# Kernel optimization log

Hardware: AMD Instinct MI355X
Metric: run time of the kernel (lower is better)

## Reference

```python
import jax, jax.numpy as jnp
import numpy as np

T, B, V, D, H, C = 2048, 32, 50257, 512, 768, 10


def setup_inputs() -> dict:
    key = jax.random.key(0)
    ks = jax.random.split(key, 11)
    s = 0.02
    return {
        "x": jax.random.randint(ks[0], (T, B), 0, V),
        "embed_table": jax.random.normal(ks[1], (V, D), jnp.float32) * s,
        "W_x": jax.random.normal(ks[2], (H, D), jnp.float32) * s,
        "W_f": jax.random.normal(ks[3], (H, D), jnp.float32) * s,
        "b_f": jax.random.normal(ks[4], (H,), jnp.float32) * s,
        "W_r": jax.random.normal(ks[5], (H, D), jnp.float32) * s,
        "b_r": jax.random.normal(ks[6], (H,), jnp.float32) * s,
        "W_cx": jax.random.normal(ks[7], (H, D), jnp.float32) * s,
        "b_cx": jax.random.normal(ks[8], (H,), jnp.float32) * s,
        "W_out": jax.random.normal(ks[9], (C, H), jnp.float32) * s,
        "b_out": jax.random.normal(ks[10], (C,), jnp.float32) * s,
    }


def reference(x, embed_table, W_x, W_f, b_f, W_r, b_r, W_cx, b_cx, W_out, b_out):
    # Embedding lookup: [T, B, D]
    e = embed_table[x]
    # Precompute all gate projections for every timestep (batched GEMMs).
    xp = jnp.einsum("tbd,hd->tbh", e, W_x)                 # x_t projection
    f = jax.nn.sigmoid(jnp.einsum("tbd,hd->tbh", e, W_f) + b_f)   # forget gate
    r = jax.nn.sigmoid(jnp.einsum("tbd,hd->tbh", e, W_r) + b_r)   # reset gate
    cx = jnp.einsum("tbd,hd->tbh", e, W_cx) + b_cx                # highway path

    c0 = jnp.zeros((B, H), e.dtype)  # init_hidden: zeros

    def step(c, inp):
        f_t, xp_t, r_t, cx_t = inp
        c = f_t * c + (1.0 - f_t) * xp_t
        h = r_t * jnp.tanh(c) + (1.0 - r_t) * cx_t
        return c, h

    _, ht = jax.lax.scan(step, c0, (f, xp, r, cx))  # ht: [T, B, H]

    # tanh -> max-pool over time -> tanh -> classifier
    pooled = jnp.max(jnp.tanh(ht), axis=0)          # [B, H]
    pooled = jnp.tanh(pooled)
    logit = pooled @ W_out.T + b_out                # [B, C]
    return logit
```

## Files before the change

### kernel.cpp

```cpp
#include <hip/hip_runtime.h>
#include <hip/hip_bf16.h>
#include <cstdint>
#include <cstddef>

#define T_DIM 2048
#define B_DIM 32
#define D_DIM 512
#define H_DIM 768
#define C_DIM 10
#define K_DIM D_DIM
#define N_DIM (4 * H_DIM)

#define TC 1024
#define NCHUNK (T_DIM / TC)
#define MC (TC * B_DIM)

#define L_SEG 64
#define S_SEG (TC / L_SEG)
#define BH (B_DIM * H_DIM)

typedef __attribute__((ext_vector_type(8))) short short8;
typedef __attribute__((ext_vector_type(4))) float float4v;

__device__ inline unsigned short f2bf(float f) {
  unsigned int u = __builtin_bit_cast(unsigned int, f);
  unsigned int r = (u + 0x7FFFu + ((u >> 16) & 1u)) >> 16;
  return (unsigned short)r;
}
__device__ inline float bf2f(unsigned short s) {
  unsigned int u = ((unsigned int)s) << 16;
  return __builtin_bit_cast(float, u);
}
__device__ inline float fast_rcp(float x) { return __builtin_amdgcn_rcpf(x); }
__device__ inline float fast_exp2(float x) { return __builtin_amdgcn_exp2f(x); }
__device__ inline float sigmoid_f(float x) {
  float e = fast_exp2(-1.4426950408889634f * x);
  return fast_rcp(1.0f + e);
}
__device__ inline float tanh_f(float x) {
  float e = fast_exp2(2.885390081777927f * x);
  return 1.0f - 2.0f * fast_rcp(e + 1.0f);
}
__device__ inline void gld16(const unsigned short* g, unsigned short* l) {
  __builtin_amdgcn_global_load_lds(
      (const __attribute__((address_space(1))) void*)g,
      (__attribute__((address_space(3))) void*)l, 16, 0, 0);
}

__global__ __launch_bounds__(256) void gather_embed_kernel(
    const int* __restrict__ x_c, const float* __restrict__ table,
    unsigned short* __restrict__ ebfc) {
  int idx = blockIdx.x * 256 + threadIdx.x;
  int m = idx >> 7;
  int k4 = (idx & 127) << 2;
  int row = x_c[m];
  float4 v = *(const float4*)(table + (size_t)row * D_DIM + k4);
  ushort4 o;
  o.x = f2bf(v.x); o.y = f2bf(v.y); o.z = f2bf(v.z); o.w = f2bf(v.w);
  *(ushort4*)(ebfc + (size_t)m * D_DIM + k4) = o;
}

__global__ __launch_bounds__(256) void convert_w_kernel(
    const float* __restrict__ Wx, const float* __restrict__ Wf,
    const float* __restrict__ Wr, const float* __restrict__ Wcx,
    unsigned short* __restrict__ wcat) {
  int idx = blockIdx.x * 256 + threadIdx.x;
  int n = idx >> 7;
  int k4 = (idx & 127) << 2;
  int mat = n / H_DIM;
  int h = n - mat * H_DIM;
  const float* src = (mat == 0) ? Wx : (mat == 1) ? Wf : (mat == 2) ? Wr : Wcx;
  float4 v = *(const float4*)(src + (size_t)h * D_DIM + k4);
  ushort4 o;
  o.x = f2bf(v.x); o.y = f2bf(v.y); o.z = f2bf(v.z); o.w = f2bf(v.w);
  *(ushort4*)(wcat + (size_t)n * D_DIM + k4) = o;
}

#define BM 128
#define BN 128
#define BK 32

__global__ __launch_bounds__(256) void gemm_kernel(
    const unsigned short* __restrict__ ebfc,
    const unsigned short* __restrict__ wcat,
    const float* __restrict__ b_f, const float* __restrict__ b_r,
    const float* __restrict__ b_cx,
    unsigned short* __restrict__ projc) {
  __shared__ __align__(16) unsigned short smem[17408];
  unsigned short* As0 = smem;
  unsigned short* As1 = smem + 4096;
  unsigned short* Bs0 = smem + 8192;
  unsigned short* Bs1 = smem + 12288;

  int tid  = threadIdx.x;
  int wave = tid >> 6;
  int lane = tid & 63;
  int quad = lane >> 4;
  int l16  = lane & 15;
  int m0 = blockIdx.y * BM;
  int n0 = blockIdx.x * BN;
  int wm = (wave >> 1) * 64;
  int wn = (wave & 1) * 64;

  int row0 = tid >> 2;
  int cl0  = (tid & 3) ^ ((row0 >> 1) & 3);
  int row1 = 64 + row0;
  int cl1  = (tid & 3) ^ ((row1 >> 1) & 3);

  float4v acc[4][4] = {};

#define STAGE(Adst, Bdst, kt) do { \
    gld16(ebfc + (size_t)(m0 + row0) * K_DIM + (kt) + cl0 * 8, (Adst) + tid * 8); \
    gld16(wcat + (size_t)(n0 + row0) * K_DIM + (kt) + cl0 * 8, (Bdst) + tid * 8); \
    gld16(ebfc + (size_t)(m0 + row1) * K_DIM + (kt) + cl1 * 8, (Adst) + 2048 + tid * 8); \
    gld16(wcat + (size_t)(n0 + row1) * K_DIM + (kt) + cl1 * 8, (Bdst) + 2048 + tid * 8); } while (0)

  STAGE(As0, Bs0, 0);
  __syncthreads();

  for (int ki = 0; ki < K_DIM / BK; ki++) {
    unsigned short* Ac = (ki & 1) ? As1 : As0;
    unsigned short* Bc = (ki & 1) ? Bs1 : Bs0;
    if (ki + 1 < K_DIM / BK) {
      unsigned short* An = (ki & 1) ? As0 : As1;
      unsigned short* Bn = (ki & 1) ? Bs0 : Bs1;
      STAGE(An, Bn, (ki + 1) * BK);
    }
    short8 af[4], bfr[4];
#pragma unroll
    for (int i = 0; i < 4; i++) {
      int r = wm + i * 16 + l16;
      int p = quad ^ ((r >> 1) & 3);
      af[i] = *(const short8*)(Ac + r * BK + p * 8);
    }
#pragma unroll
    for (int j = 0; j < 4; j++) {
      int r = wn + j * 16 + l16;
      int p = quad ^ ((r >> 1) & 3);
      bfr[j] = *(const short8*)(Bc + r * BK + p * 8);
    }
#pragma unroll
    for (int i = 0; i < 4; i++)
#pragma unroll
      for (int j = 0; j < 4; j++)
        acc[i][j] = __builtin_amdgcn_mfma_f32_16x16x32_bf16(af[i], bfr[j], acc[i][j], 0, 0, 0);
    __syncthreads();
  }

  int mat = n0 / H_DIM;
  const float* bias = (mat == 1) ? b_f : (mat == 2) ? b_r : b_cx;
#pragma unroll
  for (int i = 0; i < 4; i++) {
    int row = wm + i * 16 + quad * 4;
#pragma unroll
    for (int j = 0; j < 4; j++) {
      int col = wn + j * 16 + l16;
      int h = n0 + col - mat * H_DIM;
      float bv = (mat == 0) ? 0.0f : bias[h];
#pragma unroll
      for (int r = 0; r < 4; r++) {
        float v = acc[i][j][r] + bv;
        if (mat == 1 || mat == 2) v = sigmoid_f(v);
        smem[(row + r) * 136 + col] = f2bf(v);
      }
    }
  }
  __syncthreads();
  size_t matBase = (size_t)mat * MC * H_DIM;
  int hb = n0 - mat * H_DIM;
#pragma unroll
  for (int s = 0; s < 8; s++) {
    int idx = s * 256 + tid;
    int row = idx >> 4;
    int col8 = (idx & 15) * 8;
    short8 v = *(const short8*)(smem + row * 136 + col8);
    *(short8*)(projc + matBase + (size_t)(m0 + row) * H_DIM + hb + col8) = v;
  }
}

__global__ __launch_bounds__(128) void scan1_kernel(
    const unsigned short* __restrict__ projc,
    float* __restrict__ Pw, float* __restrict__ Qw) {
  int blk = blockIdx.x;
  int seg = blk / (B_DIM * 3);
  int rem = blk % (B_DIM * 3);
  int b = rem / 3, hc = rem % 3;
  int h = hc * 256 + threadIdx.x * 2;
  const size_t mstr = (size_t)MC * H_DIM;
  size_t idx0 = ((size_t)(seg * L_SEG) * B_DIM + b) * H_DIM + h;
  float p0 = 1.f, p1 = 1.f, c0 = 0.f, c1 = 0.f;
#pragma unroll 4
  for (int t = 0; t < L_SEG; t++) {
    size_t id = idx0 + (size_t)t * BH;
    ushort2 xp = *(const ushort2*)(projc + id);
    ushort2 ff = *(const ushort2*)(projc + mstr + id);
    float f0 = bf2f(ff.x), f1 = bf2f(ff.y);
    float x0 = bf2f(xp.x), x1 = bf2f(xp.y);
    c0 = fmaf(f0, c0 - x0, x0);
    c1 = fmaf(f1, c1 - x1, x1);
    p0 *= f0; p1 *= f1;
  }
  int o = seg * BH + b * H_DIM + h;
  *(float2*)(Pw + o) = make_float2(p0, p1);
  *(float2*)(Qw + o) = make_float2(c0, c1);
}

__global__ __launch_bounds__(256) void prefix_kernel(
    const float* __restrict__ Pw, const float* __restrict__ Qw,
    float* __restrict__ cin, float* __restrict__ c_state,
    const float* __restrict__ segmax, float* __restrict__ hm_state,
    int first, int hm_init) {
  int gid = blockIdx.x * 256 + threadIdx.x;
  float c = first ? 0.f : c_state[gid];
#pragma unroll
  for (int s = 0; s < S_SEG; s++) {
    cin[s * BH + gid] = c;
    c = fmaf(Pw[s * BH + gid], c, Qw[s * BH + gid]);
  }
  c_state[gid] = c;
  if (!first) {
    float m = segmax[gid];
#pragma unroll
    for (int s = 1; s < S_SEG; s++) m = fmaxf(m, segmax[s * BH + gid]);
    hm_state[gid] = hm_init ? m : fmaxf(hm_state[gid], m);
  }
}

__global__ __launch_bounds__(128) void scan2_kernel(
    const unsigned short* __restrict__ projc,
    const float* __restrict__ cin, float* __restrict__ segmax) {
  int blk = blockIdx.x;
  int seg = blk / (B_DIM * 3);
  int rem = blk % (B_DIM * 3);
  int b = rem / 3, hc = rem % 3;
  int h = hc * 256 + threadIdx.x * 2;
  const size_t mstr = (size_t)MC * H_DIM;
  size_t idx0 = ((size_t)(seg * L_SEG) * B_DIM + b) * H_DIM + h;
  int o = seg * BH + b * H_DIM + h;
  float2 cv = *(const float2*)(cin + o);
  float c0 = cv.x, c1 = cv.y, m0 = -1e30f, m1 = -1e30f;
#pragma unroll 4
  for (int t = 0; t < L_SEG; t++) {
    size_t id = idx0 + (size_t)t * BH;
    ushort2 xp = *(const ushort2*)(projc + id);
    ushort2 ff = *(const ushort2*)(projc + mstr + id);
    ushort2 rr = *(const ushort2*)(projc + 2 * mstr + id);
    ushort2 cx = *(const ushort2*)(projc + 3 * mstr + id);
    float f0 = bf2f(ff.x), f1 = bf2f(ff.y);
    float x0 = bf2f(xp.x), x1 = bf2f(xp.y);
    float r0 = bf2f(rr.x), r1 = bf2f(rr.y);
    float g0 = bf2f(cx.x), g1 = bf2f(cx.y);
    c0 = fmaf(f0, c0 - x0, x0);
    c1 = fmaf(f1, c1 - x1, x1);
    float h0 = fmaf(r0, tanh_f(c0) - g0, g0);
    float h1 = fmaf(r1, tanh_f(c1) - g1, g1);
    m0 = fmaxf(m0, h0); m1 = fmaxf(m1, h1);
  }
  *(float2*)(segmax + o) = make_float2(m0, m1);
}

__global__ __launch_bounds__(256) void pool_final_kernel(
    const float* __restrict__ segmax, const float* __restrict__ hm_state,
    float* __restrict__ pooled) {
  int gid = blockIdx.x * 256 + threadIdx.x;
  float m = hm_state[gid];
#pragma unroll
  for (int s = 0; s < S_SEG; s++) m = fmaxf(m, segmax[s * BH + gid]);
  pooled[gid] = tanh_f(tanh_f(m));
}

__global__ __launch_bounds__(64) void classifier_kernel(
    const float* __restrict__ pooled, const float* __restrict__ W_out,
    const float* __restrict__ b_out, float* __restrict__ out) {
  int b = blockIdx.x / C_DIM;
  int c = blockIdx.x % C_DIM;
  int lane = threadIdx.x;
  float s = 0.0f;
#pragma unroll
  for (int i = 0; i < H_DIM / 64; i++) {
    int h = i * 64 + lane;
    s += pooled[(size_t)b * H_DIM + h] * W_out[(size_t)c * H_DIM + h];
  }
#pragma unroll
  for (int off = 32; off; off >>= 1) s += __shfl_down(s, off, 64);
  if (lane == 0) out[b * C_DIM + c] = s + b_out[c];
}

extern "C" void kernel_launch(void* const* d_in, const int* in_sizes, int n_in,
                              void* d_out, int out_size, void* d_ws, size_t ws_size,
                              hipStream_t stream) {
  const int*   x     = (const int*)d_in[0];
  const float* table = (const float*)d_in[1];
  const float* W_x   = (const float*)d_in[2];
  const float* W_f   = (const float*)d_in[3];
  const float* b_f   = (const float*)d_in[4];
  const float* W_r   = (const float*)d_in[5];
  const float* b_r   = (const float*)d_in[6];
  const float* W_cx  = (const float*)d_in[7];
  const float* b_cx  = (const float*)d_in[8];
  const float* W_out = (const float*)d_in[9];
  const float* b_out = (const float*)d_in[10];

  char* ws = (char*)d_ws;
  size_t off = 0;
  unsigned short* wcat  = (unsigned short*)(ws + off); off += (size_t)N_DIM * K_DIM * 2;
  unsigned short* ebfc  = (unsigned short*)(ws + off); off += (size_t)MC * K_DIM * 2;
  unsigned short* projc = (unsigned short*)(ws + off); off += (size_t)4 * MC * H_DIM * 2;
  float* Pw     = (float*)(ws + off); off += (size_t)S_SEG * BH * 4;
  float* Qw     = (float*)(ws + off); off += (size_t)S_SEG * BH * 4;
  float* cin    = (float*)(ws + off); off += (size_t)S_SEG * BH * 4;
  float* segmax = (float*)(ws + off); off += (size_t)S_SEG * BH * 4;
  float* c_st   = (float*)(ws + off); off += (size_t)BH * 4;
  float* hm_st  = (float*)(ws + off); off += (size_t)BH * 4;
  float* pooled = (float*)(ws + off); off += (size_t)BH * 4;

  convert_w_kernel<<<(N_DIM * K_DIM / 4) / 256, 256, 0, stream>>>(W_x, W_f, W_r, W_cx, wcat);

  dim3 g(N_DIM / BN, MC / BM);
  for (int ch = 0; ch < NCHUNK; ch++) {
    gather_embed_kernel<<<(MC * K_DIM / 4) / 256, 256, 0, stream>>>(x + (size_t)ch * MC, table, ebfc);
    gemm_kernel<<<g, 256, 0, stream>>>(ebfc, wcat, b_f, b_r, b_cx, projc);
    scan1_kernel<<<S_SEG * B_DIM * 3, 128, 0, stream>>>(projc, Pw, Qw);
    prefix_kernel<<<BH / 256, 256, 0, stream>>>(Pw, Qw, cin, c_st, segmax, hm_st,
                                                ch == 0, ch == 1);
    scan2_kernel<<<S_SEG * B_DIM * 3, 128, 0, stream>>>(projc, cin, segmax);
  }
  pool_final_kernel<<<BH / 256, 256, 0, stream>>>(segmax, hm_st, pooled);
  classifier_kernel<<<B_DIM * C_DIM, 64, 0, stream>>>(pooled, W_out, b_out, (float*)d_out);
}
```

Before: 604.1 us.

## Swap MFMA operands for direct packed epilogue stores; widen scan kernels to 4 elements

The GEMM now feeds the weights as the MFMA A operand and the embeddings as B, so each lane's accumulator holds four consecutive h values. The epilogue can then add a float4 bias, apply the sigmoid and write packed 8-byte bf16 stores straight to global memory, with no LDS staging pass or extra barrier. The K loop is fully unrolled with precomputed global pointers. Both scan kernels now process four contiguous elements per thread using 8-byte loads, which halves the grid size. The direct stores are only 8 bytes and strided across rows, so they may coalesce worse than the old 16-byte row-contiguous writes.

```diff
diff --git a/kernel.cpp b/kernel.cpp
--- a/kernel.cpp
+++ b/kernel.cpp
@@ -45,6 +45,9 @@
   __builtin_amdgcn_global_load_lds(
       (const __attribute__((address_space(1))) void*)g,
       (__attribute__((address_space(3))) void*)l, 16, 0, 0);
+}
+__device__ inline unsigned int pack_bf16x2(float lo, float hi) {
+  return ((unsigned int)f2bf(hi) << 16) | (unsigned int)f2bf(lo);
 }
 
 __global__ __launch_bounds__(256) void gather_embed_kernel(
@@ -86,11 +89,8 @@
     const float* __restrict__ b_f, const float* __restrict__ b_r,
     const float* __restrict__ b_cx,
     unsigned short* __restrict__ projc) {
-  __shared__ __align__(16) unsigned short smem[17408];
-  unsigned short* As0 = smem;
-  unsigned short* As1 = smem + 4096;
-  unsigned short* Bs0 = smem + 8192;
-  unsigned short* Bs1 = smem + 12288;
+  __shared__ __align__(16) unsigned short As[2][4096];
+  __shared__ __align__(16) unsigned short Bs[2][4096];
 
   int tid  = threadIdx.x;
   int wave = tid >> 6;
@@ -99,82 +99,81 @@
   int l16  = lane & 15;
   int m0 = blockIdx.y * BM;
   int n0 = blockIdx.x * BN;
+  int wn = (wave & 1) * 64;
   int wm = (wave >> 1) * 64;
-  int wn = (wave & 1) * 64;
 
   int row0 = tid >> 2;
   int cl0  = (tid & 3) ^ ((row0 >> 1) & 3);
   int row1 = 64 + row0;
   int cl1  = (tid & 3) ^ ((row1 >> 1) & 3);
 
+  const unsigned short* gA0 = ebfc + (size_t)(m0 + row0) * K_DIM + cl0 * 8;
+  const unsigned short* gA1 = ebfc + (size_t)(m0 + row1) * K_DIM + cl1 * 8;
+  const unsigned short* gB0 = wcat + (size_t)(n0 + row0) * K_DIM + cl0 * 8;
+  const unsigned short* gB1 = wcat + (size_t)(n0 + row1) * K_DIM + cl1 * 8;
+
   float4v acc[4][4] = {};
 
-#define STAGE(Adst, Bdst, kt) do { \
-    gld16(ebfc + (size_t)(m0 + row0) * K_DIM + (kt) + cl0 * 8, (Adst) + tid * 8); \
-    gld16(wcat + (size_t)(n0 + row0) * K_DIM + (kt) + cl0 * 8, (Bdst) + tid * 8); \
-    gld16(ebfc + (size_t)(m0 + row1) * K_DIM + (kt) + cl1 * 8, (Adst) + 2048 + tid * 8); \
-    gld16(wcat + (size_t)(n0 + row1) * K_DIM + (kt) + cl1 * 8, (Bdst) + 2048 + tid * 8); } while (0)
-
-  STAGE(As0, Bs0, 0);
+#define STAGE(buf, kt) do { \
+    gld16(gA0 + (kt), As[buf] + tid * 8); \
+    gld16(gB0 + (kt), Bs[buf] + tid * 8); \
+    gld16(gA1 + (kt), As[buf] + 2048 + tid * 8); \
+    gld16(gB1 + (kt), Bs[buf] + 2048 + tid * 8); } while (0)
+
+  STAGE(0, 0);
   __syncthreads();
 
+#pragma unroll
   for (int ki = 0; ki < K_DIM / BK; ki++) {
-    unsigned short* Ac = (ki & 1) ? As1 : As0;
-    unsigned short* Bc = (ki & 1) ? Bs1 : Bs0;
-    if (ki + 1 < K_DIM / BK) {
-      unsigned short* An = (ki & 1) ? As0 : As1;
-      unsigned short* Bn = (ki & 1) ? Bs0 : Bs1;
-      STAGE(An, Bn, (ki + 1) * BK);
+    const int cur = ki & 1;
+    if (ki + 1 < K_DIM / BK) STAGE(cur ^ 1, (ki + 1) * BK);
+    short8 wf[4], ef[4];
+#pragma unroll
+    for (int i = 0; i < 4; i++) {
+      int r = wn + i * 16 + l16;
+      int p = quad ^ ((r >> 1) & 3);
+      wf[i] = *(const short8*)(Bs[cur] + r * BK + p * 8);
     }
-    short8 af[4], bfr[4];
-#pragma unroll
-    for (int i = 0; i < 4; i++) {
-      int r = wm + i * 16 + l16;
+#pragma unroll
+    for (int j = 0; j < 4; j++) {
+      int r = wm + j * 16 + l16;
       int p = quad ^ ((r >> 1) & 3);
-      af[i] = *(const short8*)(Ac + r * BK + p * 8);
+      ef[j] = *(const short8*)(As[cur] + r * BK + p * 8);
     }
 #pragma unroll
+    for (int i = 0; i < 4; i++)
+#pragma unroll
+      for (int j = 0; j < 4; j++)
+        acc[i][j] = __builtin_amdgcn_mfma_f32_16x16x32_bf16(wf[i], ef[j], acc[i][j], 0, 0, 0);
+    __syncthreads();
+  }
+
+  int mat = n0 / H_DIM;
+  int hb = n0 - mat * H_DIM;
+  size_t matBase = (size_t)mat * MC * H_DIM;
+  const float* bias = (mat == 1) ? b_f : (mat == 2) ? b_r : b_cx;
+#pragma unroll
+  for (int i = 0; i < 4; i++) {
+    int h0 = hb + wn + i * 16 + quad * 4;
+    float4 bv;
+    if (mat == 0) { bv.x = bv.y = bv.z = bv.w = 0.0f; }
+    else          { bv = *(const float4*)(bias + h0); }
+#pragma unroll
     for (int j = 0; j < 4; j++) {
-      int r = wn + j * 16 + l16;
-      int p = quad ^ ((r >> 1) & 3);
-      bfr[j] = *(const short8*)(Bc + r * BK + p * 8);
+      int m = m0 + wm + j * 16 + l16;
+      float v0 = acc[i][j][0] + bv.x;
+      float v1 = acc[i][j][1] + bv.y;
+      float v2 = acc[i][j][2] + bv.z;
+      float v3 = acc[i][j][3] + bv.w;
+      if (mat == 1 || mat == 2) {
+        v0 = sigmoid_f(v0); v1 = sigmoid_f(v1);
+        v2 = sigmoid_f(v2); v3 = sigmoid_f(v3);
+      }
+      uint2 pk;
+      pk.x = pack_bf16x2(v0, v1);
+      pk.y = pack_bf16x2(v2, v3);
+      *(uint2*)(projc + matBase + (size_t)m * H_DIM + h0) = pk;
     }
-#pragma unroll
-    for (int i = 0; i < 4; i++)
-#pragma unroll
-      for (int j = 0; j < 4; j++)
-        acc[i][j] = __builtin_amdgcn_mfma_f32_16x16x32_bf16(af[i], bfr[j], acc[i][j], 0, 0, 0);
-    __syncthreads();
-  }
-
-  int mat = n0 / H_DIM;
-  const float* bias = (mat == 1) ? b_f : (mat == 2) ? b_r : b_cx;
-#pragma unroll
-  for (int i = 0; i < 4; i++) {
-    int row = wm + i * 16 + quad * 4;
-#pragma unroll
-    for (int j = 0; j < 4; j++) {
-      int col = wn + j * 16 + l16;
-      int h = n0 + col - mat * H_DIM;
-      float bv = (mat == 0) ? 0.0f : bias[h];
-#pragma unroll
-      for (int r = 0; r < 4; r++) {
-        float v = acc[i][j][r] + bv;
-        if (mat == 1 || mat == 2) v = sigmoid_f(v);
-        smem[(row + r) * 136 + col] = f2bf(v);
-      }
-    }
-  }
-  __syncthreads();
-  size_t matBase = (size_t)mat * MC * H_DIM;
-  int hb = n0 - mat * H_DIM;
-#pragma unroll
-  for (int s = 0; s < 8; s++) {
-    int idx = s * 256 + tid;
-    int row = idx >> 4;
-    int col8 = (idx & 15) * 8;
-    short8 v = *(const short8*)(smem + row * 136 + col8);
-    *(short8*)(projc + matBase + (size_t)(m0 + row) * H_DIM + hb + col8) = v;
   }
 }
 
@@ -182,27 +181,28 @@
     const unsigned short* __restrict__ projc,
     float* __restrict__ Pw, float* __restrict__ Qw) {
   int blk = blockIdx.x;
-  int seg = blk / (B_DIM * 3);
-  int rem = blk % (B_DIM * 3);
-  int b = rem / 3, hc = rem % 3;
-  int h = hc * 256 + threadIdx.x * 2;
+  int seg = blk / (BH / 512);
+  int q   = blk % (BH / 512);
+  int e4  = (q * 128 + threadIdx.x) * 4;
   const size_t mstr = (size_t)MC * H_DIM;
-  size_t idx0 = ((size_t)(seg * L_SEG) * B_DIM + b) * H_DIM + h;
-  float p0 = 1.f, p1 = 1.f, c0 = 0.f, c1 = 0.f;
+  size_t idx0 = (size_t)(seg * L_SEG) * BH + e4;
+  float p0 = 1.f, p1 = 1.f, p2 = 1.f, p3 = 1.f;
+  float c0 = 0.f, c1 = 0.f, c2 = 0.f, c3 = 0.f;
 #pragma unroll 4
   for (int t = 0; t < L_SEG; t++) {
     size_t id = idx0 + (size_t)t * BH;
-    ushort2 xp = *(const ushort2*)(projc + id);
-    ushort2 ff = *(const ushort2*)(projc + mstr + id);
-    float f0 = bf2f(ff.x), f1 = bf2f(ff.y);
-    float x0 = bf2f(xp.x), x1 = bf2f(xp.y);
-    c0 = fmaf(f0, c0 - x0, x0);
-    c1 = fmaf(f1, c1 - x1, x1);
-    p0 *= f0; p1 *= f1;
-  }
-  int o = seg * BH + b * H_DIM + h;
-  *(float2*)(Pw + o) = make_float2(p0, p1);
-  *(float2*)(Qw + o) = make_float2(c0, c1);
+    ushort4 xp = *(const ushort4*)(projc + id);
+    ushort4 ff = *(const ushort4*)(projc + mstr + id);
+    float f0 = bf2f(ff.x), f1 = bf2f(ff.y), f2 = bf2f(ff.z), f3 = bf2f(ff.w);
+    c0 = fmaf(f0, c0 - bf2f(xp.x), bf2f(xp.x));
+    c1 = fmaf(f1, c1 - bf2f(xp.y), bf2f(xp.y));
+    c2 = fmaf(f2, c2 - bf2f(xp.z), bf2f(xp.z));
+    c3 = fmaf(f3, c3 - bf2f(xp.w), bf2f(xp.w));
+    p0 *= f0; p1 *= f1; p2 *= f2; p3 *= f3;
+  }
+  int o = seg * BH + e4;
+  *(float4*)(Pw + o) = make_float4(p0, p1, p2, p3);
+  *(float4*)(Qw + o) = make_float4(c0, c1, c2, c3);
 }
 
 __global__ __launch_bounds__(256) void prefix_kernel(
@@ -230,33 +230,34 @@
     const unsigned short* __restrict__ projc,
     const float* __restrict__ cin, float* __restrict__ segmax) {
   int blk = blockIdx.x;
-  int seg = blk / (B_DIM * 3);
-  int rem = blk % (B_DIM * 3);
-  int b = rem / 3, hc = rem % 3;
-  int h = hc * 256 + threadIdx.x * 2;
+  int seg = blk / (BH / 512);
+  int q   = blk % (BH / 512);
+  int e4  = (q * 128 + threadIdx.x) * 4;
   const size_t mstr = (size_t)MC * H_DIM;
-  size_t idx0 = ((size_t)(seg * L_SEG) * B_DIM + b) * H_DIM + h;
-  int o = seg * BH + b * H_DIM + h;
-  float2 cv = *(const float2*)(cin + o);
-  float c0 = cv.x, c1 = cv.y, m0 = -1e30f, m1 = -1e30f;
-#pragma unroll 4
+  size_t idx0 = (size_t)(seg * L_SEG) * BH + e4;
+  int o = seg * BH + e4;
+  float4 cv = *(const float4*)(cin + o);
+  float c0 = cv.x, c1 = cv.y, c2 = cv.z, c3 = cv.w;
+  float m0 = -1e30f, m1 = -1e30f, m2 = -1e30f, m3 = -1e30f;
+#pragma unroll 2
   for (int t = 0; t < L_SEG; t++) {
     size_t id = idx0 + (size_t)t * BH;
-    ushort2 xp = *(const ushort2*)(projc + id);
-    ushort2 ff = *(const ushort2*)(projc + mstr + id);
-    ushort2 rr = *(const ushort2*)(projc + 2 * mstr + id);
-    ushort2 cx = *(const ushort2*)(projc + 3 * mstr + id);
-    float f0 = bf2f(ff.x), f1 = bf2f(ff.y);
-    float x0 = bf2f(xp.x), x1 = bf2f(xp.y);
-    float r0 = bf2f(rr.x), r1 = bf2f(rr.y);
-    float g0 = bf2f(cx.x), g1 = bf2f(cx.y);
-    c0 = fmaf(f0, c0 - x0, x0);
-    c1 = fmaf(f1, c1 - x1, x1);
-    float h0 = fmaf(r0, tanh_f(c0) - g0, g0);
-    float h1 = fmaf(r1, tanh_f(c1) - g1, g1);
+    ushort4 xp = *(const ushort4*)(projc + id);
+    ushort4 ff = *(const ushort4*)(projc + mstr + id);
+    ushort4 rr = *(const ushort4*)(projc + 2 * mstr + id);
+    ushort4 cx = *(const ushort4*)(projc + 3 * mstr + id);
+    c0 = fmaf(bf2f(ff.x), c0 - bf2f(xp.x), bf2f(xp.x));
+    c1 = fmaf(bf2f(ff.y), c1 - bf2f(xp.y), bf2f(xp.y));
+    c2 = fmaf(bf2f(ff.z), c2 - bf2f(xp.z), bf2f(xp.z));
+    c3 = fmaf(bf2f(ff.w), c3 - bf2f(xp.w), bf2f(xp.w));
+    float h0 = fmaf(bf2f(rr.x), tanh_f(c0) - bf2f(cx.x), bf2f(cx.x));
+    float h1 = fmaf(bf2f(rr.y), tanh_f(c1) - bf2f(cx.y), bf2f(cx.y));
+    float h2 = fmaf(bf2f(rr.z), tanh_f(c2) - bf2f(cx.z), bf2f(cx.z));
+    float h3 = fmaf(bf2f(rr.w), tanh_f(c3) - bf2f(cx.w), bf2f(cx.w));
     m0 = fmaxf(m0, h0); m1 = fmaxf(m1, h1);
-  }
-  *(float2*)(segmax + o) = make_float2(m0, m1);
+    m2 = fmaxf(m2, h2); m3 = fmaxf(m3, h3);
+  }
+  *(float4*)(segmax + o) = make_float4(m0, m1, m2, m3);
 }
 
 __global__ __launch_bounds__(256) void pool_final_kernel(
@@ -320,10 +321,10 @@
   for (int ch = 0; ch < NCHUNK; ch++) {
     gather_embed_kernel<<<(MC * K_DIM / 4) / 256, 256, 0, stream>>>(x + (size_t)ch * MC, table, ebfc);
     gemm_kernel<<<g, 256, 0, stream>>>(ebfc, wcat, b_f, b_r, b_cx, projc);
-    scan1_kernel<<<S_SEG * B_DIM * 3, 128, 0, stream>>>(projc, Pw, Qw);
+    scan1_kernel<<<S_SEG * (BH / 512), 128, 0, stream>>>(projc, Pw, Qw);
     prefix_kernel<<<BH / 256, 256, 0, stream>>>(Pw, Qw, cin, c_st, segmax, hm_st,
                                                 ch == 0, ch == 1);
-    scan2_kernel<<<S_SEG * B_DIM * 3, 128, 0, stream>>>(projc, cin, segmax);
+    scan2_kernel<<<S_SEG * (BH / 512), 128, 0, stream>>>(projc, cin, segmax);
   }
   pool_final_kernel<<<BH / 256, 256, 0, stream>>>(segmax, hm_st, pooled);
   classifier_kernel<<<B_DIM * C_DIM, 64, 0, stream>>>(pooled, W_out, b_out, (float*)d_out);
```

Result: no change. 610.2 us (+1.0%).
